# Kernel optimization log

Hardware: AMD Instinct MI355X
Metric: run time of the kernel (lower is better)

The kernel has to match this reference:

```python
import jax, jax.numpy as jnp
import numpy as np

B, S, H, NH, DH, DFF = 4, 8192, 2048, 16, 128, 8192
K = 1024
EPS = 1e-5
THETA = 10000.0
SCALE_FACTOR = 1.0
SCALE_GAP = 1.0


def setup_inputs() -> dict:
    key = jax.random.key(0)
    ks = jax.random.split(key, 12)
    hidden_states = jax.random.normal(ks[0], (B, S, H), dtype=jnp.float32)
    position_ids = jnp.broadcast_to(jnp.arange(S, dtype=jnp.int32)[None, :], (B, S))
    # exactly K routed tokens per row -> static compacted length (matches torch
    # path when all rows have equal top-k counts)
    rowkeys = jax.random.split(ks[1], B)
    sel = jax.vmap(lambda k: jax.random.permutation(k, S)[:K])(rowkeys)  # [B,K]
    topk_mask = jnp.zeros((B, S), dtype=bool).at[jnp.arange(B)[:, None], sel].set(True)
    topk_scores = jax.random.uniform(ks[2], (B,), dtype=jnp.float32)
    w = lambda k, shp: (jax.random.normal(k, shp, dtype=jnp.float32) * 0.02)
    return {
        "hidden_states": hidden_states,
        "position_ids": position_ids,
        "topk_mask": topk_mask,
        "topk_scores": topk_scores,
        "topk_k": K,
        "Wq": w(ks[3], (H, H)),
        "Wk": w(ks[4], (H, H)),
        "Wv": w(ks[5], (H, H)),
        "Wo": w(ks[6], (H, H)),
        "Wgate": w(ks[7], (H, DFF)),
        "Wup": w(ks[8], (H, DFF)),
        "Wdown": w(ks[9], (DFF, H)),
        "ln1_w": jnp.ones((H,), dtype=jnp.float32),
        "ln2_w": jnp.ones((H,), dtype=jnp.float32),
    }


def _rmsnorm(x, w):
    return x * jax.lax.rsqrt(jnp.mean(x * x, axis=-1, keepdims=True) + EPS) * w


def _rotate_half(x):
    x1, x2 = jnp.split(x, 2, axis=-1)
    return jnp.concatenate([-x2, x1], axis=-1)


def reference(hidden_states, position_ids, topk_mask, topk_scores, topk_k,
              Wq, Wk, Wv, Wo, Wgate, Wup, Wdown, ln1_w, ln2_w):
    Kk = int(topk_k)
    b, s, h = hidden_states.shape
    # true positions first, in original order (stable) -> compacted indices
    order = jnp.argsort(jnp.where(topk_mask, 0, 1).astype(jnp.int32), axis=1, stable=True)
    topk_idx = order[:, :Kk]                              # [B,K]
    bidx = jnp.arange(b)[:, None]
    # 🔍 dispatch: gather routed tokens into compact [B,K,H]
    x = hidden_states[bidx, topk_idx]
    pos = position_ids[bidx, topk_idx]                    # original positions for RoPE

    residual = x
    hs = _rmsnorm(x, ln1_w)
    q = (hs @ Wq).reshape(b, Kk, NH, DH).transpose(0, 2, 1, 3)
    k = (hs @ Wk).reshape(b, Kk, NH, DH).transpose(0, 2, 1, 3)
    v = (hs @ Wv).reshape(b, Kk, NH, DH).transpose(0, 2, 1, 3)
    inv_freq = 1.0 / (THETA ** (jnp.arange(0, DH, 2, dtype=jnp.float32) / DH))
    freqs = pos[..., None].astype(jnp.float32) * inv_freq  # [B,K,DH/2]
    emb = jnp.concatenate([freqs, freqs], axis=-1)
    cos = jnp.cos(emb)[:, None, :, :]
    sin = jnp.sin(emb)[:, None, :, :]
    q = q * cos + _rotate_half(q) * sin
    k = k * cos + _rotate_half(k) * sin
    scores = jnp.einsum('bhqd,bhkd->bhqk', q, k) / np.sqrt(DH).astype(np.float32)
    causal = jnp.tril(jnp.ones((Kk, Kk), dtype=bool))
    scores = jnp.where(causal, scores, jnp.finfo(scores.dtype).min)
    attn = jax.nn.softmax(scores, axis=-1)
    o = jnp.einsum('bhqk,bhkd->bhqd', attn, v).transpose(0, 2, 1, 3).reshape(b, Kk, H)
    hs = residual + o @ Wo

    residual2 = hs
    m = _rmsnorm(hs, ln2_w)
    m = (jax.nn.silu(m @ Wgate) * (m @ Wup)) @ Wdown

    # rescale_hidden_states=True path
    scale = 0.5 * SCALE_FACTOR + (topk_scores - 0.5) * SCALE_GAP  # [B]
    out_gathered = residual2 + m * scale[:, None, None]
    # 🔍 combine: scatter routed outputs back; bottom tokens pass through unchanged
    out = hidden_states.at[bidx, topk_idx].set(out_gathered)
    return out
```

## Files before the change

### kernel.cpp

```cpp
#include <hip/hip_runtime.h>
#include <hip/hip_bf16.h>
#include <stdint.h>

#define Bb 4
#define Ss 8192
#define Hh 2048
#define NHh 16
#define DHh 128
#define DFFf 8192
#define KS 1024
#define NTOK 4096

typedef unsigned short u16;
typedef __bf16 bf16x8 __attribute__((ext_vector_type(8)));
typedef float f32x4 __attribute__((ext_vector_type(4)));

union B8 { uint4 u; bf16x8 v; u16 s[8]; };

__device__ __forceinline__ float b2f(u16 x) { return __uint_as_float(((unsigned)x) << 16); }
__device__ __forceinline__ u16 f2b(float x) {
  __hip_bfloat16 h = __float2bfloat16(x);
  return *reinterpret_cast<u16*>(&h);
}

__device__ __forceinline__ void gll16(const void* g, void* l) {
  __builtin_amdgcn_global_load_lds((const __attribute__((address_space(1))) void*)g,
                                   (__attribute__((address_space(3))) void*)l, 16, 0, 0);
}

__device__ __forceinline__ int swz16(int r, int cg) {
  int u = ((r & 1) << 2) | cg;
  return ((r >> 1) << 3) | (u ^ ((r >> 1) & 7));
}

__global__ void topk_prep(const void* maskp, const int* __restrict__ posids,
                          const float* __restrict__ scores,
                          int* __restrict__ idx, int* __restrict__ posg,
                          float* __restrict__ scalev) {
  int b = blockIdx.x;
  int tid = threadIdx.x, lane = tid & 63, wv = tid >> 6;
  __shared__ int wsum[4];
  __shared__ int base;
  __shared__ int mode;
  __shared__ int detCnt;
  if (tid == 0) { base = 0; detCnt = 0; }
  __syncthreads();
  {
    const unsigned char* mb = (const unsigned char*)maskp;
    int c = 0;
    for (int s = tid; s < 8192; s += 256) c += (mb[s] != 0);
    atomicAdd(&detCnt, c);
  }
  __syncthreads();
  if (tid == 0) mode = (detCnt == KS) ? 1 : 0;
  __syncthreads();
  const unsigned char* mb = (const unsigned char*)maskp;
  const int* mi = (const int*)maskp;
  for (int s0 = 0; s0 < Ss; s0 += 256) {
    int s = s0 + tid;
    int pred = mode ? (mb[(size_t)b * Ss + s] != 0) : (mi[(size_t)b * Ss + s] != 0);
    unsigned long long bal = __ballot(pred);
    int lp = __popcll(bal & ((1ull << lane) - 1ull));
    int wtot = __popcll(bal);
    if (lane == 0) wsum[wv] = wtot;
    __syncthreads();
    int woff = 0;
    for (int w = 0; w < wv; ++w) woff += wsum[w];
    int tot = wsum[0] + wsum[1] + wsum[2] + wsum[3];
    int p = base + woff + lp;
    if (pred && p < KS) {
      idx[b * KS + p] = s;
      posg[b * KS + p] = posids[(size_t)b * Ss + s];
    }
    __syncthreads();
    if (tid == 0) base += tot;
    __syncthreads();
  }
  if (b == 0 && tid < Bb) scalev[tid] = 0.5f * 1.0f + (scores[tid] - 0.5f) * 1.0f;
}

__global__ void transpose_w(const float* __restrict__ in, u16* __restrict__ out, int R, int C) {
  __shared__ float tile[32][33];
  int tx = threadIdx.x, ty = threadIdx.y;
  int c0 = blockIdx.x * 32, r0 = blockIdx.y * 32;
  for (int j = ty; j < 32; j += 8) tile[j][tx] = in[(size_t)(r0 + j) * C + c0 + tx];
  __syncthreads();
  for (int j = ty; j < 32; j += 8) out[(size_t)(c0 + j) * R + r0 + tx] = f2b(tile[tx][j]);
}

template <int GATHER>
__global__ __launch_bounds__(256) void rmsnorm_k(const float* __restrict__ src0,
                                                 const int* __restrict__ idx,
                                                 const float* __restrict__ w,
                                                 u16* __restrict__ out) {
  int t = blockIdx.x;
  const float* src;
  if (GATHER) { int b = t >> 10; src = src0 + ((size_t)b * Ss + idx[t]) * Hh; }
  else src = src0 + (size_t)t * Hh;
  int tid = threadIdx.x, lane = tid & 63, wv = tid >> 6;
  float4 x0 = *(const float4*)(src + tid * 8);
  float4 x1 = *(const float4*)(src + tid * 8 + 4);
  float ss = x0.x * x0.x + x0.y * x0.y + x0.z * x0.z + x0.w * x0.w +
             x1.x * x1.x + x1.y * x1.y + x1.z * x1.z + x1.w * x1.w;
  for (int o = 32; o; o >>= 1) ss += __shfl_down(ss, o);
  __shared__ float wred[4];
  if (lane == 0) wred[wv] = ss;
  __syncthreads();
  float tot = wred[0] + wred[1] + wred[2] + wred[3];
  float r = rsqrtf(tot * (1.0f / Hh) + 1e-5f);
  const float* wp = w + tid * 8;
  u16* op = out + (size_t)t * Hh + tid * 8;
  float xs[8] = {x0.x, x0.y, x0.z, x0.w, x1.x, x1.y, x1.z, x1.w};
#pragma unroll
  for (int j = 0; j < 8; ++j) op[j] = f2b(xs[j] * r * wp[j]);
}

template <int EPI>
__global__ __launch_bounds__(512, 2) void gemm256(
    const u16* __restrict__ A, const u16* __restrict__ Bt,
    int N, int Kd, int lda, int gm, int gw,
    u16* __restrict__ Cb,
    const float* __restrict__ hid, const int* __restrict__ idx,
    const float* __restrict__ hs2, const float* __restrict__ scalev,
    float* __restrict__ Cf) {
  __shared__ u16 lds[65536];
  int bid = blockIdx.x;
  int xcd = bid & 7;
  int i2 = bid >> 3;
  int bm = i2 / gw;
  int bn = xcd * gw + i2 % gw;
  int m0 = bm * 256, n0 = bn * 256;
  int tid = threadIdx.x, lane = tid & 63, wv = tid >> 6;
  int wm = wv >> 2, wn = wv & 3;
  int NT = Kd >> 6;

  int P16 = wv * 64 + lane;
  int blk = P16 >> 3, up = P16 & 7;
  int uu = up ^ (blk & 7);
  int r0 = blk * 2 + (uu >> 2), cg0 = uu & 3;
  const u16* srcA = A + (size_t)(m0 + r0) * lda + cg0 * 8;
  const u16* srcB = Bt + (size_t)(n0 + r0) * Kd + cg0 * 8;
  size_t rsA = (size_t)128 * lda, rsB = (size_t)128 * Kd;

  int offA = swz16(wm * 128 + (lane & 15), lane >> 4) * 8;
  int offB = 32768 + swz16(wn * 64 + (lane & 15), lane >> 4) * 8;
  u16* ldsw = &lds[wv * 512];

  f32x4 acc[8][4] = {};
  B8 aR[4], bR[4];

  gll16(srcB,      ldsw + 32768); gll16(srcB + rsB,      ldsw + 36864);
  gll16(srcA,      ldsw +     0); gll16(srcA + rsA,      ldsw +  4096);
  gll16(srcB + 32, ldsw + 40960); gll16(srcB + 32 + rsB, ldsw + 45056);
  gll16(srcA + 32, ldsw +  8192); gll16(srcA + 32 + rsA, ldsw + 12288);
  gll16(srcB + 64, ldsw + 49152); gll16(srcB + 64 + rsB, ldsw + 53248);
  gll16(srcA + 64, ldsw + 16384); gll16(srcA + 64 + rsA, ldsw + 20480);
  gll16(srcB + 96, ldsw + 57344); gll16(srcB + 96 + rsB, ldsw + 61440);
  asm volatile("s_waitcnt vmcnt(6)" ::: "memory");
  asm volatile("s_barrier" ::: "memory");

  const u16* stA = srcA + 64;
  const u16* stB = srcB + 64;

  auto phase = [&](int abase, int bbase, int mh) {
    if (mh == 0) {
#pragma unroll
      for (int nf = 0; nf < 4; ++nf) bR[nf].u = *(const uint4*)&lds[offB + bbase + nf * 512];
    }
#pragma unroll
    for (int i3 = 0; i3 < 4; ++i3)
      aR[i3].u = *(const uint4*)&lds[offA + abase + (i3 + 4 * mh) * 512];
  };
  auto mfma16 = [&](int mh) {
    asm volatile("s_barrier" ::: "memory");
    asm volatile("s_waitcnt lgkmcnt(0)" ::: "memory");
    __builtin_amdgcn_s_setprio(1);
#pragma unroll
    for (int nf = 0; nf < 4; ++nf)
#pragma unroll
      for (int i3 = 0; i3 < 4; ++i3)
        acc[mh * 4 + i3][nf] =
            __builtin_amdgcn_mfma_f32_16x16x32_bf16(aR[i3].v, bR[nf].v, acc[mh * 4 + i3][nf], 0, 0, 0);
    __builtin_amdgcn_s_setprio(0);
  };

  for (int ktp = 0; ktp < NT; ktp += 2) {
    bool sAll = (ktp < NT - 2);
    phase(0, 0, 0);
    { gll16(stA + 32, ldsw + 24576); gll16(stA + 32 + rsA, ldsw + 28672); }
    mfma16(0);
    asm volatile("s_barrier" ::: "memory");
    phase(0, 0, 1);
    if (sAll) { gll16(stB + 64, ldsw + 32768); gll16(stB + 64 + rsB, ldsw + 36864); }
    mfma16(1);
    asm volatile("s_barrier" ::: "memory");
    phase(8192, 8192, 0);
    if (sAll) { gll16(stA + 64, ldsw + 0); gll16(stA + 64 + rsA, ldsw + 4096); }
    mfma16(0);
    asm volatile("s_barrier" ::: "memory");
    phase(8192, 8192, 1);
    if (sAll) { gll16(stB + 96, ldsw + 40960); gll16(stB + 96 + rsB, ldsw + 45056); }
    mfma16(1);
    if (sAll) asm volatile("s_waitcnt vmcnt(6)" ::: "memory");
    else asm volatile("s_waitcnt vmcnt(0)" ::: "memory");
    asm volatile("s_barrier" ::: "memory");
    phase(16384, 16384, 0);
    if (sAll) { gll16(stA + 96, ldsw + 8192); gll16(stA + 96 + rsA, ldsw + 12288); }
    mfma16(0);
    asm volatile("s_barrier" ::: "memory");
    phase(16384, 16384, 1);
    if (sAll) { gll16(stB + 128, ldsw + 49152); gll16(stB + 128 + rsB, ldsw + 53248); }
    mfma16(1);
    asm volatile("s_barrier" ::: "memory");
    phase(24576, 24576, 0);
    if (sAll) { gll16(stA + 128, ldsw + 16384); gll16(stA + 128 + rsA, ldsw + 20480); }
    mfma16(0);
    asm volatile("s_barrier" ::: "memory");
    phase(24576, 24576, 1);
    if (sAll) { gll16(stB + 160, ldsw + 57344); gll16(stB + 160 + rsB, ldsw + 61440); }
    mfma16(1);
    if (sAll) asm volatile("s_waitcnt vmcnt(6)" ::: "memory");
    asm volatile("s_barrier" ::: "memory");
    stA += 128; stB += 128;
  }

#pragma unroll
  for (int mf = 0; mf < 8; ++mf) {
#pragma unroll
    for (int rr = 0; rr < 4; ++rr) {
      int row = m0 + wm * 128 + mf * 16 + (lane >> 4) * 4 + rr;
#pragma unroll
      for (int nf = 0; nf < 4; ++nf) {
        int col = n0 + wn * 64 + nf * 16 + (lane & 15);
        float v = acc[mf][nf][rr];
        if (EPI == 0) {
          Cb[(size_t)row * N + col] = f2b(v);
        } else if (EPI == 1) {
          int b = row >> 10;
          Cf[(size_t)row * Hh + col] = hid[((size_t)b * Ss + idx[row]) * Hh + col] + v;
        } else {
          int b = row >> 10;
          Cf[((size_t)b * Ss + idx[row]) * Hh + col] = hs2[(size_t)row * Hh + col] + v * scalev[b];
        }
      }
    }
  }
}

template <int EPI>
__global__ __launch_bounds__(512, 2) void gemm128(
    const u16* __restrict__ A, const u16* __restrict__ Bt,
    int N, int Kd, int lda, int gm, int gw,
    u16* __restrict__ Cb,
    const float* __restrict__ hid, const int* __restrict__ idx,
    const float* __restrict__ hs2, const float* __restrict__ scalev,
    float* __restrict__ Cf, u16* __restrict__ vTout) {
  __shared__ u16 lds[49152];
  int bid = blockIdx.x;
  int xcd = bid & 7;
  int i2 = bid >> 3;
  int bm = i2 / gw;
  int bn = xcd * gw + i2 % gw;
  int m0 = bm * 128, n0 = bn * 256;
  int tid = threadIdx.x, lane = tid & 63, wv = tid >> 6;
  int wm = wv >> 2, wn = wv & 3;
  int NT = Kd >> 6;

  int P16 = wv * 64 + lane;
  int blk = P16 >> 3, up = P16 & 7;
  int uu = up ^ (blk & 7);
  int r0 = blk * 2 + (uu >> 2), cg0 = uu & 3;
  const u16* srcA = A + (size_t)(m0 + r0) * lda + cg0 * 8;
  const u16* srcB = Bt + (size_t)(n0 + r0) * Kd + cg0 * 8;
  size_t rsB = (size_t)128 * Kd;

  int offB = swz16(wn * 64 + (lane & 15), lane >> 4) * 8;
  int offA = 32768 + swz16(wm * 64 + (lane & 15), lane >> 4) * 8;
  u16* ldsw = &lds[wv * 512];

  f32x4 acc[4][4] = {};
  B8 aR[4], bR[4];

  gll16(srcB,      ldsw +     0); gll16(srcB + rsB,      ldsw +  4096); gll16(srcA,      ldsw + 32768);
  gll16(srcB + 32, ldsw +  8192); gll16(srcB + 32 + rsB, ldsw + 12288); gll16(srcA + 32, ldsw + 36864);
  gll16(srcB + 64, ldsw + 16384); gll16(srcB + 64 + rsB, ldsw + 20480); gll16(srcA + 64, ldsw + 40960);
  asm volatile("s_waitcnt vmcnt(6)" ::: "memory");
  asm volatile("s_barrier" ::: "memory");

  const u16* stA = srcA + 64;
  const u16* stB = srcB + 64;

  auto rd = [&](int s) {
#pragma unroll
    for (int f = 0; f < 4; ++f) bR[f].u = *(const uint4*)&lds[offB + s * 8192 + f * 512];
#pragma unroll
    for (int f = 0; f < 4; ++f) aR[f].u = *(const uint4*)&lds[offA + s * 4096 + f * 512];
  };
  auto mfma16 = [&]() {
    asm volatile("s_barrier" ::: "memory");
    asm volatile("s_waitcnt lgkmcnt(0)" ::: "memory");
    __builtin_amdgcn_s_setprio(1);
#pragma unroll
    for (int nf = 0; nf < 4; ++nf)
#pragma unroll
      for (int mf = 0; mf < 4; ++mf)
        acc[mf][nf] = __builtin_amdgcn_mfma_f32_16x16x32_bf16(aR[mf].v, bR[nf].v, acc[mf][nf], 0, 0, 0);
    __builtin_amdgcn_s_setprio(0);
  };

  for (int ktp = 0; ktp < NT; ktp += 2) {
    bool sAll = (ktp < NT - 2);
    rd(0);
    { gll16(stB + 32, ldsw + 24576); gll16(stB + 32 + rsB, ldsw + 28672); gll16(stA + 32, ldsw + 45056); }
    mfma16();
    asm volatile("s_waitcnt vmcnt(6)" ::: "memory");
    asm volatile("s_barrier" ::: "memory");
    rd(1);
    if (sAll) { gll16(stB + 64, ldsw + 0); gll16(stB + 64 + rsB, ldsw + 4096); gll16(stA + 64, ldsw + 32768); }
    mfma16();
    if (sAll) asm volatile("s_waitcnt vmcnt(6)" ::: "memory");
    else asm volatile("s_waitcnt vmcnt(3)" ::: "memory");
    asm volatile("s_barrier" ::: "memory");
    rd(2);
    if (sAll) { gll16(stB + 96, ldsw + 8192); gll16(stB + 96 + rsB, ldsw + 12288); gll16(stA + 96, ldsw + 36864); }
    mfma16();
    if (sAll) asm volatile("s_waitcnt vmcnt(6)" ::: "memory");
    else asm volatile("s_waitcnt vmcnt(0)" ::: "memory");
    asm volatile("s_barrier" ::: "memory");
    rd(3);
    if (sAll) { gll16(stB + 128, ldsw + 16384); gll16(stB + 128 + rsB, ldsw + 20480); gll16(stA + 128, ldsw + 40960); }
    mfma16();
    if (sAll) asm volatile("s_waitcnt vmcnt(6)" ::: "memory");
    asm volatile("s_barrier" ::: "memory");
    stA += 128; stB += 128;
  }

  if (EPI == 3) {
#pragma unroll
    for (int mf = 0; mf < 4; ++mf) {
      int rowb = m0 + wm * 64 + mf * 16 + (lane >> 4) * 4;
      int bb = rowb >> 10, kk2 = rowb & 1023;
#pragma unroll
      for (int nf = 0; nf < 4; ++nf) {
        int col = n0 + wn * 64 + nf * 16 + (lane & 15);
        if (col >= 4096) {
          int hh = (col - 4096) >> 7, dd = (col - 4096) & 127;
          ushort4 pk;
          pk.x = f2b(acc[mf][nf][0]); pk.y = f2b(acc[mf][nf][1]);
          pk.z = f2b(acc[mf][nf][2]); pk.w = f2b(acc[mf][nf][3]);
          *(ushort4*)&vTout[(((size_t)bb * 16 + hh) * 128 + dd) * 1024 + kk2] = pk;
        } else {
#pragma unroll
          for (int rr = 0; rr < 4; ++rr)
            Cb[(size_t)(rowb + rr) * N + col] = f2b(acc[mf][nf][rr]);
        }
      }
    }
    return;
  }

#pragma unroll
  for (int mf = 0; mf < 4; ++mf) {
#pragma unroll
    for (int rr = 0; rr < 4; ++rr) {
      int row = m0 + wm * 64 + mf * 16 + (lane >> 4) * 4 + rr;
#pragma unroll
      for (int nf = 0; nf < 4; ++nf) {
        int col = n0 + wn * 64 + nf * 16 + (lane & 15);
        float v = acc[mf][nf][rr];
        if (EPI == 0) {
          Cb[(size_t)row * N + col] = f2b(v);
        } else if (EPI == 1) {
          int b = row >> 10;
          Cf[(size_t)row * Hh + col] = hid[((size_t)b * Ss + idx[row]) * Hh + col] + v;
        } else {
          int b = row >> 10;
          Cf[((size_t)b * Ss + idx[row]) * Hh + col] = hs2[(size_t)row * Hh + col] + v * scalev[b];
        }
      }
    }
  }
}

__global__ __launch_bounds__(256) void rope_qk(u16* __restrict__ qkv,
                                               const int* __restrict__ posg) {
  int gid = blockIdx.x * 256 + threadIdx.x;
  int i = gid & 63;
  int h = (gid >> 6) & 15;
  int t = gid >> 10;
  float p = (float)posg[t];
  float inv = exp2f(-(float)i * (13.287712379549449f / 64.0f));
  float ang = p * inv;
  float sv, cv;
  sincosf(ang, &sv, &cv);
  size_t base = (size_t)t * 6144 + h * DHh + i;
  u16* Q = qkv;
  u16* Kq = qkv + 2048;
  float q1 = b2f(Q[base]), q2 = b2f(Q[base + 64]);
  Q[base] = f2b(q1 * cv - q2 * sv);
  Q[base + 64] = f2b(q2 * cv + q1 * sv);
  float k1 = b2f(Kq[base]), k2 = b2f(Kq[base + 64]);
  Kq[base] = f2b(k1 * cv - k2 * sv);
  Kq[base + 64] = f2b(k2 * cv + k1 * sv);
}

__global__ __launch_bounds__(256) void attn_k(const u16* __restrict__ QKV,
                                              const u16* __restrict__ vT,
                                              u16* __restrict__ O) {
  int qb = blockIdx.x;
  int head = blockIdx.y;
  int b = head >> 4, h = head & 15;
  int tid = threadIdx.x, lane = tid & 63, wv = tid >> 6;
  int l15 = lane & 15, lq = lane >> 4, l7 = lane & 7;
  __shared__ __align__(16) u16 KsA[8192];
  __shared__ __align__(16) u16 VtA[8192];
  u16* PsB = &KsA[wv * 1152];

  int key0 = tid >> 4;
  int uK = (tid & 15) ^ (key0 & 7);
  int koff = key0 * 6144 + uK * 8;
  int d0s = tid >> 3;
  int uV = (tid & 7) ^ (d0s & 7);
  size_t voffB = ((size_t)head * 128 + d0s) * 1024 + uV * 8;
  char* dK = (char*)KsA + wv * 1024;
  char* dV = (char*)VtA + wv * 1024;

  int q0 = qb * 64 + wv * 16;
  int tokQ = b * KS + q0;
  B8 qf[4];
  const u16* qp = QKV + (size_t)(tokQ + l15) * 6144 + h * DHh;
#pragma unroll
  for (int c = 0; c < 4; ++c) qf[c].u = *(const uint4*)(qp + c * 32 + lq * 8);
  float m_run = -1e30f, l_run = 0.0f;
  f32x4 oacc[8] = {};
  int qi = q0 + l15;

  for (int ks = 0; ks <= qb * 64; ks += 64) {
    bool maskTile = (ks == qb * 64);
    __syncthreads();
    const u16* kp = QKV + (size_t)(b * KS + ks) * 6144 + 2048 + h * DHh;
    const u16* vp = vT + voffB + ks;
    gll16(kp + koff,          dK);
    gll16(kp + koff +  98304, dK + 4096);
    gll16(kp + koff + 196608, dK + 8192);
    gll16(kp + koff + 294912, dK + 12288);
    gll16(vp,          dV);
    gll16(vp + 32768,  dV + 4096);
    gll16(vp + 65536,  dV + 8192);
    gll16(vp + 98304,  dV + 12288);
    asm volatile("s_waitcnt vmcnt(0)" ::: "memory");
    __syncthreads();
    f32x4 st[4] = {};
#pragma unroll
    for (int c = 0; c < 4; ++c) {
#pragma unroll
      for (int kt = 0; kt < 4; ++kt) {
        B8 kf;
        kf.u = *(const uint4*)&KsA[(kt * 16 + l15) * 128 + (((c * 4 + lq) ^ l7) * 8)];
        st[kt] = __builtin_amdgcn_mfma_f32_16x16x32_bf16(kf.v, qf[c].v, st[kt], 0, 0, 0);
      }
    }
    __syncthreads();
    float pmax = -INFINITY;
    if (maskTile) {
#pragma unroll
      for (int kt = 0; kt < 4; ++kt)
#pragma unroll
        for (int r = 0; r < 4; ++r) {
          int ki = ks + kt * 16 + lq * 4 + r;
          float v = st[kt][r] * 0.088388347648318447f;
          v = (ki <= qi) ? v : -INFINITY;
          st[kt][r] = v;
          pmax = fmaxf(pmax, v);
        }
    } else {
#pragma unroll
      for (int kt = 0; kt < 4; ++kt)
#pragma unroll
        for (int r = 0; r < 4; ++r) {
          float v = st[kt][r] * 0.088388347648318447f;
          st[kt][r] = v;
          pmax = fmaxf(pmax, v);
        }
    }
    pmax = fmaxf(pmax, __shfl_xor(pmax, 16));
    pmax = fmaxf(pmax, __shfl_xor(pmax, 32));
    float m_new = fmaxf(m_run, pmax);
    float alpha = __expf(m_run - m_new);
    float psum = 0.0f;
#pragma unroll
    for (int kt = 0; kt < 4; ++kt)
#pragma unroll
      for (int r = 0; r < 4; ++r) {
        float pv = __expf(st[kt][r] - m_new);
        st[kt][r] = pv;
        psum += pv;
      }
    psum += __shfl_xor(psum, 16);
    psum += __shfl_xor(psum, 32);
    l_run = l_run * alpha + psum;
    m_run = m_new;
#pragma unroll
    for (int kt = 0; kt < 4; ++kt) {
      ushort4 pk;
      pk.x = f2b(st[kt][0]); pk.y = f2b(st[kt][1]);
      pk.z = f2b(st[kt][2]); pk.w = f2b(st[kt][3]);
      *(ushort4*)&PsB[l15 * 72 + kt * 16 + lq * 4] = pk;
    }
    B8 pf0, pf1;
    pf0.u = *(const uint4*)&PsB[l15 * 72 + lq * 8];
    pf1.u = *(const uint4*)&PsB[l15 * 72 + 32 + lq * 8];
    float al0 = __shfl(alpha, lq * 4 + 0);
    float al1 = __shfl(alpha, lq * 4 + 1);
    float al2 = __shfl(alpha, lq * 4 + 2);
    float al3 = __shfl(alpha, lq * 4 + 3);
#pragma unroll
    for (int dt = 0; dt < 8; ++dt) {
      oacc[dt][0] *= al0; oacc[dt][1] *= al1;
      oacc[dt][2] *= al2; oacc[dt][3] *= al3;
    }
#pragma unroll
    for (int dt = 0; dt < 8; ++dt) {
      int d = dt * 16 + l15;
      B8 vf;
      vf.u = *(const uint4*)&VtA[d * 64 + ((lq ^ l7) * 8)];
      oacc[dt] = __builtin_amdgcn_mfma_f32_16x16x32_bf16(pf0.v, vf.v, oacc[dt], 0, 0, 0);
      vf.u = *(const uint4*)&VtA[d * 64 + (((4 + lq) ^ l7) * 8)];
      oacc[dt] = __builtin_amdgcn_mfma_f32_16x16x32_bf16(pf1.v, vf.v, oacc[dt], 0, 0, 0);
    }
  }
  float linv = 1.0f / l_run;
  float li[4];
#pragma unroll
  for (int r = 0; r < 4; ++r) li[r] = __shfl(linv, lq * 4 + r);
#pragma unroll
  for (int r = 0; r < 4; ++r) {
    int tok = tokQ + lq * 4 + r;
    u16* op = O + (size_t)tok * Hh + h * DHh;
#pragma unroll
    for (int dt = 0; dt < 8; ++dt) op[dt * 16 + l15] = f2b(oacc[dt][r] * li[r]);
  }
}

__global__ __launch_bounds__(256) void silu_gu(u16* __restrict__ gu) {
  size_t gid = (size_t)blockIdx.x * 256 + threadIdx.x;
  size_t t = gid >> 10;
  int c = (int)(gid & 1023) * 8;
  u16* gp = gu + t * 16384 + c;
  const u16* upp = gp + 8192;
  B8 gv, uv;
  gv.u = *(const uint4*)gp;
  uv.u = *(const uint4*)upp;
#pragma unroll
  for (int j = 0; j < 8; ++j) {
    float x = b2f(gv.s[j]), y = b2f(uv.s[j]);
    gv.s[j] = f2b(x / (1.0f + __expf(-x)) * y);
  }
  *(uint4*)gp = gv.u;
}

extern "C" void kernel_launch(void* const* d_in, const int* in_sizes, int n_in,
                              void* d_out, int out_size, void* d_ws, size_t ws_size,
                              hipStream_t stream) {
  (void)in_sizes; (void)n_in; (void)out_size; (void)ws_size;
  const float* hid = (const float*)d_in[0];
  const int* posids = (const int*)d_in[1];
  const void* mask = d_in[2];
  const float* scores = (const float*)d_in[3];
  const float* Wq = (const float*)d_in[5];
  const float* Wk = (const float*)d_in[6];
  const float* Wv = (const float*)d_in[7];
  const float* Wo = (const float*)d_in[8];
  const float* Wg = (const float*)d_in[9];
  const float* Wu = (const float*)d_in[10];
  const float* Wd = (const float*)d_in[11];
  const float* ln1 = (const float*)d_in[12];
  const float* ln2 = (const float*)d_in[13];
  float* out = (float*)d_out;
  char* ws = (char*)d_ws;

  u16* WqkvT = (u16*)(ws + 0);
  u16* WoT   = (u16*)(ws + 25165824);
  u16* WguT  = (u16*)(ws + 33554432);
  u16* WdT   = (u16*)(ws + 100663296);
  int* idx   = (int*)(ws + 134217728);
  int* posg  = (int*)(ws + 134217728 + 16384);
  float* scalev = (float*)(ws + 134217728 + 32768);
  char* R = ws + 134283264;
  u16* hsn    = (u16*)(R);
  u16* qkv    = (u16*)(R + 16777216);
  u16* attn_o = (u16*)(R + 67108864);
  u16* vT     = (u16*)(R + 88080384);
  u16* gu     = (u16*)(R);
  float* hs2  = (float*)(ws + 268500992);
  u16* mnorm  = (u16*)(ws + 302055424);

  hipMemcpyAsync(out, hid, (size_t)Bb * Ss * Hh * 4, hipMemcpyDeviceToDevice, stream);

  topk_prep<<<Bb, 256, 0, stream>>>(mask, posids, scores, idx, posg, scalev);

  transpose_w<<<dim3(64, 64), dim3(32, 8), 0, stream>>>(Wq, WqkvT, 2048, 2048);
  transpose_w<<<dim3(64, 64), dim3(32, 8), 0, stream>>>(Wk, WqkvT + 2048 * 2048, 2048, 2048);
  transpose_w<<<dim3(64, 64), dim3(32, 8), 0, stream>>>(Wv, WqkvT + 4096 * 2048, 2048, 2048);
  transpose_w<<<dim3(64, 64), dim3(32, 8), 0, stream>>>(Wo, WoT, 2048, 2048);
  transpose_w<<<dim3(256, 64), dim3(32, 8), 0, stream>>>(Wg, WguT, 2048, 8192);
  transpose_w<<<dim3(256, 64), dim3(32, 8), 0, stream>>>(Wu, WguT + 8192 * 2048, 2048, 8192);
  transpose_w<<<dim3(64, 256), dim3(32, 8), 0, stream>>>(Wd, WdT, 8192, 2048);

  rmsnorm_k<1><<<NTOK, 256, 0, stream>>>(hid, idx, ln1, hsn);

  gemm128<3><<<768, 512, 0, stream>>>(hsn, WqkvT, 6144, 2048, 2048, 32, 3, qkv,
                                      nullptr, nullptr, nullptr, nullptr, nullptr, vT);

  rope_qk<<<16384, 256, 0, stream>>>(qkv, posg);

  attn_k<<<dim3(16, 64), 256, 0, stream>>>(qkv, vT, attn_o);

  gemm128<1><<<256, 512, 0, stream>>>(attn_o, WoT, 2048, 2048, 2048, 32, 1, nullptr,
                                      hid, idx, nullptr, nullptr, hs2, nullptr);

  rmsnorm_k<0><<<NTOK, 256, 0, stream>>>(hs2, nullptr, ln2, mnorm);

  gemm256<0><<<1024, 512, 0, stream>>>(mnorm, WguT, 16384, 2048, 2048, 16, 8, gu,
                                       nullptr, nullptr, nullptr, nullptr, nullptr);

  silu_gu<<<16384, 256, 0, stream>>>(gu);

  gemm128<2><<<256, 512, 0, stream>>>(gu, WdT, 2048, 8192, 16384, 32, 1, nullptr,
                                      nullptr, idx, hs2, scalev, out, nullptr);
}
```

Measured before the change: 1.178 ms.

## Fuse SiLU-gate into gate/up GEMM epilogue and widen attention key tiles

Interleaves the gate and up weight columns in 32-column groups so each gemm256 tile holds matching gate/up accumulators. A new epilogue then writes silu(g)*u directly as an 8192-wide bf16 buffer, which removes the separate silu kernel and halves the intermediate the down projection has to read. Separately, the attention kernel now processes 128-key tiles instead of 64, doubling the LDS buffers to cut loop iterations and barriers at the cost of more LDS and registers. RoPE also switches to the fast __sincosf intrinsic, which loses accuracy for large angles.

```diff
diff --git a/kernel.cpp b/kernel.cpp
--- a/kernel.cpp
+++ b/kernel.cpp
@@ -79,13 +79,18 @@
   if (b == 0 && tid < Bb) scalev[tid] = 0.5f * 1.0f + (scores[tid] - 0.5f) * 1.0f;
 }
 
+template <int MODE>
 __global__ void transpose_w(const float* __restrict__ in, u16* __restrict__ out, int R, int C) {
   __shared__ float tile[32][33];
   int tx = threadIdx.x, ty = threadIdx.y;
   int c0 = blockIdx.x * 32, r0 = blockIdx.y * 32;
   for (int j = ty; j < 32; j += 8) tile[j][tx] = in[(size_t)(r0 + j) * C + c0 + tx];
   __syncthreads();
-  for (int j = ty; j < 32; j += 8) out[(size_t)(c0 + j) * R + r0 + tx] = f2b(tile[tx][j]);
+  for (int j = ty; j < 32; j += 8) {
+    int c = c0 + j;
+    size_t row = (MODE == 0) ? c : (size_t)((c >> 5) << 6) + (c & 31) + (MODE == 2 ? 32 : 0);
+    out[row * R + r0 + tx] = f2b(tile[tx][j]);
+  }
 }
 
 template <int GATHER>
@@ -224,6 +229,24 @@
     stA += 128; stB += 128;
   }
 
+  if (EPI == 4) {
+    int gcol0 = ((n0 + wn * 64) >> 1) + (lane & 15);
+#pragma unroll
+    for (int mf = 0; mf < 8; ++mf) {
+#pragma unroll
+      for (int rr = 0; rr < 4; ++rr) {
+        int row = m0 + wm * 128 + mf * 16 + (lane >> 4) * 4 + rr;
+#pragma unroll
+        for (int nf = 0; nf < 2; ++nf) {
+          float g = acc[mf][nf][rr];
+          float u = acc[mf][nf + 2][rr];
+          Cb[(size_t)row * 8192 + gcol0 + nf * 16] = f2b(g / (1.0f + __expf(-g)) * u);
+        }
+      }
+    }
+    return;
+  }
+
 #pragma unroll
   for (int mf = 0; mf < 8; ++mf) {
 #pragma unroll
@@ -392,7 +415,7 @@
   float inv = exp2f(-(float)i * (13.287712379549449f / 64.0f));
   float ang = p * inv;
   float sv, cv;
-  sincosf(ang, &sv, &cv);
+  __sincosf(ang, &sv, &cv);
   size_t base = (size_t)t * 6144 + h * DHh + i;
   u16* Q = qkv;
   u16* Kq = qkv + 2048;
@@ -412,16 +435,14 @@
   int b = head >> 4, h = head & 15;
   int tid = threadIdx.x, lane = tid & 63, wv = tid >> 6;
   int l15 = lane & 15, lq = lane >> 4, l7 = lane & 7;
-  __shared__ __align__(16) u16 KsA[8192];
-  __shared__ __align__(16) u16 VtA[8192];
-  u16* PsB = &KsA[wv * 1152];
-
-  int key0 = tid >> 4;
-  int uK = (tid & 15) ^ (key0 & 7);
-  int koff = key0 * 6144 + uK * 8;
-  int d0s = tid >> 3;
-  int uV = (tid & 7) ^ (d0s & 7);
-  size_t voffB = ((size_t)head * 128 + d0s) * 1024 + uV * 8;
+  __shared__ __align__(16) u16 KsA[16384];
+  __shared__ __align__(16) u16 VtA[16384];
+  u16* PsB = &KsA[wv * 2176];
+
+  int keyr = tid >> 4;
+  int uphys = tid & 15;
+  size_t koff0 = (size_t)keyr * 6144 + ((uphys ^ (keyr & 7)) * 8);
+  size_t voff0 = (size_t)keyr * 1024 + ((uphys ^ (keyr & 7)) * 8);
   char* dK = (char*)KsA + wv * 1024;
   char* dV = (char*)VtA + wv * 1024;
 
@@ -435,26 +456,25 @@
   f32x4 oacc[8] = {};
   int qi = q0 + l15;
 
-  for (int ks = 0; ks <= qb * 64; ks += 64) {
-    bool maskTile = (ks == qb * 64);
+  int nt = (qb >> 1) + 1;
+  for (int t = 0; t < nt; ++t) {
+    int ks = t * 128;
+    bool maskTile = (t == nt - 1);
     __syncthreads();
-    const u16* kp = QKV + (size_t)(b * KS + ks) * 6144 + 2048 + h * DHh;
-    const u16* vp = vT + voffB + ks;
-    gll16(kp + koff,          dK);
-    gll16(kp + koff +  98304, dK + 4096);
-    gll16(kp + koff + 196608, dK + 8192);
-    gll16(kp + koff + 294912, dK + 12288);
-    gll16(vp,          dV);
-    gll16(vp + 32768,  dV + 4096);
-    gll16(vp + 65536,  dV + 8192);
-    gll16(vp + 98304,  dV + 12288);
+    const u16* kp = QKV + (size_t)(b * KS + ks) * 6144 + 2048 + h * DHh + koff0;
+    const u16* vp = vT + ((size_t)head * 128) * 1024 + ks + voff0;
+#pragma unroll
+    for (int i = 0; i < 8; ++i) {
+      gll16(kp + (size_t)i * 16 * 6144, dK + i * 4096);
+      gll16(vp + (size_t)i * 16 * 1024, dV + i * 4096);
+    }
     asm volatile("s_waitcnt vmcnt(0)" ::: "memory");
     __syncthreads();
-    f32x4 st[4] = {};
+    f32x4 st[8] = {};
 #pragma unroll
     for (int c = 0; c < 4; ++c) {
 #pragma unroll
-      for (int kt = 0; kt < 4; ++kt) {
+      for (int kt = 0; kt < 8; ++kt) {
         B8 kf;
         kf.u = *(const uint4*)&KsA[(kt * 16 + l15) * 128 + (((c * 4 + lq) ^ l7) * 8)];
         st[kt] = __builtin_amdgcn_mfma_f32_16x16x32_bf16(kf.v, qf[c].v, st[kt], 0, 0, 0);
@@ -464,7 +484,7 @@
     float pmax = -INFINITY;
     if (maskTile) {
 #pragma unroll
-      for (int kt = 0; kt < 4; ++kt)
+      for (int kt = 0; kt < 8; ++kt)
 #pragma unroll
         for (int r = 0; r < 4; ++r) {
           int ki = ks + kt * 16 + lq * 4 + r;
@@ -475,7 +495,7 @@
         }
     } else {
 #pragma unroll
-      for (int kt = 0; kt < 4; ++kt)
+      for (int kt = 0; kt < 8; ++kt)
 #pragma unroll
         for (int r = 0; r < 4; ++r) {
           float v = st[kt][r] * 0.088388347648318447f;
@@ -489,7 +509,7 @@
     float alpha = __expf(m_run - m_new);
     float psum = 0.0f;
 #pragma unroll
-    for (int kt = 0; kt < 4; ++kt)
+    for (int kt = 0; kt < 8; ++kt)
 #pragma unroll
       for (int r = 0; r < 4; ++r) {
         float pv = __expf(st[kt][r] - m_new);
@@ -501,15 +521,16 @@
     l_run = l_run * alpha + psum;
     m_run = m_new;
 #pragma unroll
-    for (int kt = 0; kt < 4; ++kt) {
+    for (int kt = 0; kt < 8; ++kt) {
       ushort4 pk;
       pk.x = f2b(st[kt][0]); pk.y = f2b(st[kt][1]);
       pk.z = f2b(st[kt][2]); pk.w = f2b(st[kt][3]);
-      *(ushort4*)&PsB[l15 * 72 + kt * 16 + lq * 4] = pk;
-    }
-    B8 pf0, pf1;
-    pf0.u = *(const uint4*)&PsB[l15 * 72 + lq * 8];
-    pf1.u = *(const uint4*)&PsB[l15 * 72 + 32 + lq * 8];
+      *(ushort4*)&PsB[l15 * 136 + kt * 16 + lq * 4] = pk;
+    }
+    B8 pf[4];
+#pragma unroll
+    for (int kslot = 0; kslot < 4; ++kslot)
+      pf[kslot].u = *(const uint4*)&PsB[l15 * 136 + kslot * 32 + lq * 8];
     float al0 = __shfl(alpha, lq * 4 + 0);
     float al1 = __shfl(alpha, lq * 4 + 1);
     float al2 = __shfl(alpha, lq * 4 + 2);
@@ -522,11 +543,12 @@
 #pragma unroll
     for (int dt = 0; dt < 8; ++dt) {
       int d = dt * 16 + l15;
-      B8 vf;
-      vf.u = *(const uint4*)&VtA[d * 64 + ((lq ^ l7) * 8)];
-      oacc[dt] = __builtin_amdgcn_mfma_f32_16x16x32_bf16(pf0.v, vf.v, oacc[dt], 0, 0, 0);
-      vf.u = *(const uint4*)&VtA[d * 64 + (((4 + lq) ^ l7) * 8)];
-      oacc[dt] = __builtin_amdgcn_mfma_f32_16x16x32_bf16(pf1.v, vf.v, oacc[dt], 0, 0, 0);
+#pragma unroll
+      for (int kslot = 0; kslot < 4; ++kslot) {
+        B8 vf;
+        vf.u = *(const uint4*)&VtA[d * 128 + (((kslot * 4 + lq) ^ l7) * 8)];
+        oacc[dt] = __builtin_amdgcn_mfma_f32_16x16x32_bf16(pf[kslot].v, vf.v, oacc[dt], 0, 0, 0);
+      }
     }
   }
   float linv = 1.0f / l_run;
@@ -540,23 +562,6 @@
 #pragma unroll
     for (int dt = 0; dt < 8; ++dt) op[dt * 16 + l15] = f2b(oacc[dt][r] * li[r]);
   }
-}
-
-__global__ __launch_bounds__(256) void silu_gu(u16* __restrict__ gu) {
-  size_t gid = (size_t)blockIdx.x * 256 + threadIdx.x;
-  size_t t = gid >> 10;
-  int c = (int)(gid & 1023) * 8;
-  u16* gp = gu + t * 16384 + c;
-  const u16* upp = gp + 8192;
-  B8 gv, uv;
-  gv.u = *(const uint4*)gp;
-  uv.u = *(const uint4*)upp;
-#pragma unroll
-  for (int j = 0; j < 8; ++j) {
-    float x = b2f(gv.s[j]), y = b2f(uv.s[j]);
-    gv.s[j] = f2b(x / (1.0f + __expf(-x)) * y);
-  }
-  *(uint4*)gp = gv.u;
 }
 
 extern "C" void kernel_launch(void* const* d_in, const int* in_sizes, int n_in,
@@ -591,7 +596,7 @@
   u16* qkv    = (u16*)(R + 16777216);
   u16* attn_o = (u16*)(R + 67108864);
   u16* vT     = (u16*)(R + 88080384);
-  u16* gu     = (u16*)(R);
+  u16* gu2    = (u16*)(R);
   float* hs2  = (float*)(ws + 268500992);
   u16* mnorm  = (u16*)(ws + 302055424);
 
@@ -599,13 +604,13 @@
 
   topk_prep<<<Bb, 256, 0, stream>>>(mask, posids, scores, idx, posg, scalev);
 
-  transpose_w<<<dim3(64, 64), dim3(32, 8), 0, stream>>>(Wq, WqkvT, 2048, 2048);
-  transpose_w<<<dim3(64, 64), dim3(32, 8), 0, stream>>>(Wk, WqkvT + 2048 * 2048, 2048, 2048);
-  transpose_w<<<dim3(64, 64), dim3(32, 8), 0, stream>>>(Wv, WqkvT + 4096 * 2048, 2048, 2048);
-  transpose_w<<<dim3(64, 64), dim3(32, 8), 0, stream>>>(Wo, WoT, 2048, 2048);
-  transpose_w<<<dim3(256, 64), dim3(32, 8), 0, stream>>>(Wg, WguT, 2048, 8192);
-  transpose_w<<<dim3(256, 64), dim3(32, 8), 0, stream>>>(Wu, WguT + 8192 * 2048, 2048, 8192);
-  transpose_w<<<dim3(64, 256), dim3(32, 8), 0, stream>>>(Wd, WdT, 8192, 2048);
+  transpose_w<0><<<dim3(64, 64), dim3(32, 8), 0, stream>>>(Wq, WqkvT, 2048, 2048);
+  transpose_w<0><<<dim3(64, 64), dim3(32, 8), 0, stream>>>(Wk, WqkvT + 2048 * 2048, 2048, 2048);
+  transpose_w<0><<<dim3(64, 64), dim3(32, 8), 0, stream>>>(Wv, WqkvT + 4096 * 2048, 2048, 2048);
+  transpose_w<0><<<dim3(64, 64), dim3(32, 8), 0, stream>>>(Wo, WoT, 2048, 2048);
+  transpose_w<1><<<dim3(256, 64), dim3(32, 8), 0, stream>>>(Wg, WguT, 2048, 8192);
+  transpose_w<2><<<dim3(256, 64), dim3(32, 8), 0, stream>>>(Wu, WguT, 2048, 8192);
+  transpose_w<0><<<dim3(64, 256), dim3(32, 8), 0, stream>>>(Wd, WdT, 8192, 2048);
 
   rmsnorm_k<1><<<NTOK, 256, 0, stream>>>(hid, idx, ln1, hsn);
 
@@ -621,11 +626,9 @@
 
   rmsnorm_k<0><<<NTOK, 256, 0, stream>>>(hs2, nullptr, ln2, mnorm);
 
-  gemm256<0><<<1024, 512, 0, stream>>>(mnorm, WguT, 16384, 2048, 2048, 16, 8, gu,
+  gemm256<4><<<1024, 512, 0, stream>>>(mnorm, WguT, 16384, 2048, 2048, 16, 8, gu2,
                                        nullptr, nullptr, nullptr, nullptr, nullptr);
 
-  silu_gu<<<16384, 256, 0, stream>>>(gu);
-
-  gemm128<2><<<256, 512, 0, stream>>>(gu, WdT, 2048, 8192, 16384, 32, 1, nullptr,
+  gemm128<2><<<256, 512, 0, stream>>>(gu2, WdT, 2048, 8192, 8192, 32, 1, nullptr,
                                       nullptr, idx, hs2, scalev, out, nullptr);
 }
```

After: 1.076 ms. 1.1x faster.
